# Kernel optimization log

Hardware: AMD Instinct MI355X
Metric: run time of the kernel (lower is better)

The kernel has to match this reference:

```python
import jax, jax.numpy as jnp
import numpy as np

SKIP_THRESHOLD = 0.3
NUM_HEADS = 16
TOP_K = 2


def _layernorm(x, g, b, eps=1e-6):
    m = jnp.mean(x, axis=-1, keepdims=True)
    v = jnp.var(x, axis=-1, keepdims=True)
    return (x - m) * jax.lax.rsqrt(v + eps) * g + b


def _silu(x):
    return x * jax.nn.sigmoid(x)


def _causal_dwconv(x, w):
    # x: [B,S,C], w: [k,C] depthwise causal conv
    k, S = w.shape[0], x.shape[1]
    xp = jnp.pad(x, ((0, 0), (k - 1, 0), (0, 0)))
    return sum(xp[:, i:i + S, :] * w[i] for i in range(k))


def _same_dwconv(x, w):
    k, S = w.shape[0], x.shape[1]
    pl = k // 2
    xp = jnp.pad(x, ((0, 0), (pl, k - 1 - pl), (0, 0)))
    return sum(xp[:, i:i + S, :] * w[i] for i in range(k))


def _mamba_block(x, w_in, conv_w, a_log, w_bc, w_dt, dt_bias, d_skip, w_out):
    # Selective-scan SSM (Mamba-style), O(L)
    B, S, D = x.shape
    d_inner = conv_w.shape[1]
    n = w_bc.shape[1] // 2
    xz = x @ w_in                                   # [B,S,2*d_inner]
    xc, z = xz[..., :d_inner], xz[..., d_inner:]
    xc = _silu(_causal_dwconv(xc, conv_w))
    bc = xc @ w_bc                                  # [B,S,2n]
    Bt, Ct = bc[..., :n], bc[..., n:]
    dt = jax.nn.softplus(xc * w_dt + dt_bias)       # [B,S,d_inner]
    A = -jnp.exp(a_log)                             # [d_inner]

    def step(h, inp):
        xc_t, dt_t, B_t, C_t = inp                  # [B,d_inner],[B,d_inner],[B,n],[B,n]
        decay = jnp.exp(dt_t * A)[..., None]        # [B,d_inner,1]
        h = decay * h + (dt_t * xc_t)[..., None] * B_t[:, None, :]
        y_t = jnp.einsum('bcn,bn->bc', h, C_t)
        return h, y_t

    h0 = jnp.zeros((B, d_inner, n), x.dtype)
    xs = (xc.transpose(1, 0, 2), dt.transpose(1, 0, 2),
          Bt.transpose(1, 0, 2), Ct.transpose(1, 0, 2))
    _, ys = jax.lax.scan(step, h0, xs)
    y = ys.transpose(1, 0, 2) + d_skip * xc
    return (y * _silu(z)) @ w_out


def _timecrystal_block(x, theta, w, b):
    # Energy-conserving rotation-style mixing
    return jnp.cos(theta) * x + jnp.sin(theta) * jnp.tanh(x @ w + b)


def _wlam_block(x, wq, wk, wv, wo, conv_w, nh):
    # Haar wavelet decomposition -> attention on approx coeffs -> reconstruct
    B, S, D = x.shape
    hd = D // nh
    inv = 0.7071067811865476
    xe, xo = x[:, 0::2], x[:, 1::2]
    a = (xe + xo) * inv                             # approx [B,S/2,D]
    det = (xe - xo) * inv                           # detail
    L = a.shape[1]
    q = (a @ wq).reshape(B, L, nh, hd)
    k = (a @ wk).reshape(B, L, nh, hd)
    v = (a @ wv).reshape(B, L, nh, hd)
    att = jnp.einsum('bqhd,bkhd->bhqk', q, k) * (1.0 / np.sqrt(hd))
    att = jax.nn.softmax(att, axis=-1)
    o = jnp.einsum('bhqk,bkhd->bqhd', att, v).reshape(B, L, D) @ wo
    xe2 = (o + det) * inv
    xo2 = (o - det) * inv
    y = jnp.stack([xe2, xo2], axis=2).reshape(B, S, D)
    return _same_dwconv(y, conv_w)


def _moe_block(x, wg, w1, b1, w2, b2, top_k):
    # Top-k sparse MoE; dense per-expert compute weighted by top-k gates
    B, S, D = x.shape
    E = wg.shape[1]
    xt = x.reshape(-1, D)
    logits = xt @ wg
    topv, topi = jax.lax.top_k(logits, top_k)
    w = jax.nn.softmax(topv, axis=-1)
    gates = (jax.nn.one_hot(topi, E, dtype=x.dtype) * w[..., None]).sum(axis=1)  # [T,E]
    y = jnp.zeros_like(xt)
    for e in range(E):
        h = jax.nn.gelu(xt @ w1[e] + b1[e])
        y = y + gates[:, e:e + 1] * (h @ w2[e] + b2[e])
    return y.reshape(B, S, D)


def setup_inputs() -> dict:
    key = jax.random.key(0)
    ks = jax.random.split(key, 20)
    B, S, D = 2, 2048, 1024
    DI, N, CK = 2 * D, 64, 4
    E, FF = 8, 4096
    NB = 4

    def rn(k, shape, scale=0.02):
        return jax.random.normal(k, shape, dtype=jnp.float32) * scale

    return {
        'hidden_states': jax.random.normal(ks[0], (B, S, D), jnp.float32),
        'router_w': rn(ks[1], (D, NB)),
        'router_b': jnp.zeros((NB,), jnp.float32),
        'ln_g': jnp.ones((NB, D), jnp.float32),
        'ln_b': jnp.zeros((NB, D), jnp.float32),
        'm_win': rn(ks[2], (D, 2 * DI)),
        'm_conv': rn(ks[3], (CK, DI), 0.1),
        'm_alog': jnp.zeros((DI,), jnp.float32),
        'm_wbc': rn(ks[4], (DI, 2 * N)),
        'm_wdt': rn(ks[5], (DI,)),
        'm_dtb': jnp.full((DI,), -1.0, jnp.float32),
        'm_dskip': jnp.ones((DI,), jnp.float32),
        'm_wout': rn(ks[6], (DI, D)),
        'tc_theta': jnp.array(0.5, jnp.float32),
        'tc_w': rn(ks[7], (D, D)),
        'tc_b': jnp.zeros((D,), jnp.float32),
        'w_q': rn(ks[8], (D, D)),
        'w_k': rn(ks[9], (D, D)),
        'w_v': rn(ks[10], (D, D)),
        'w_o': rn(ks[11], (D, D)),
        'wlam_conv': rn(ks[12], (4, D), 0.25),
        'moe_wg': rn(ks[13], (D, E)),
        'moe_w1': rn(ks[14], (E, D, FF)),
        'moe_b1': jnp.zeros((E, FF), jnp.float32),
        'moe_w2': rn(ks[15], (E, FF, D)),
        'moe_b2': jnp.zeros((E, D), jnp.float32),
    }


def reference(hidden_states, router_w, router_b, ln_g, ln_b,
              m_win, m_conv, m_alog, m_wbc, m_wdt, m_dtb, m_dskip, m_wout,
              tc_theta, tc_w, tc_b,
              w_q, w_k, w_v, w_o, wlam_conv,
              moe_wg, moe_w1, moe_b1, moe_w2, moe_b2):
    h = hidden_states
    # Adaptive block router: mean pool -> sigmoid scores -> hard skip mask (inference)
    pooled = jnp.mean(h, axis=1)                     # [B,D]
    scores = jax.nn.sigmoid(pooled @ router_w + router_b)  # [B,4]
    masks = (scores > SKIP_THRESHOLD).astype(h.dtype)

    h = h + masks[:, 0, None, None] * _mamba_block(
        _layernorm(h, ln_g[0], ln_b[0]), m_win, m_conv, m_alog, m_wbc,
        m_wdt, m_dtb, m_dskip, m_wout)
    h = h + masks[:, 1, None, None] * _timecrystal_block(
        _layernorm(h, ln_g[1], ln_b[1]), tc_theta, tc_w, tc_b)
    h = h + masks[:, 2, None, None] * _wlam_block(
        _layernorm(h, ln_g[2], ln_b[2]), w_q, w_k, w_v, w_o, wlam_conv, NUM_HEADS)
    h = h + masks[:, 3, None, None] * _moe_block(
        _layernorm(h, ln_g[3], ln_b[3]), moe_wg, moe_w1, moe_b1, moe_w2, moe_b2, TOP_K)
    return h
```

## Files before the change

### kernel.cpp

```cpp
#include <hip/hip_runtime.h>
#include <math.h>

#define S_LEN   2048
#define B_SZ    2
#define DM      1024
#define DI      2048
#define NST     64
#define LH      1024
#define NH      16
#define HD      64
#define TT      4096
#define NEXP    8
#define FF      4096
#define CHK     1024
#define MAXTILE 72
#define INVR2   0.7071067811865476f
#define CHUNK   128
#define NCH     16

#define OFF_POOLED 0
#define OFF_COUNTS 2048
#define OFF_CURSOR 2056
#define OFF_MASKS  2064
#define OFF_NTILE  2072
// ... 17 lines not shown
#define MB_HB   0
#define MB_W1T  4194304
#define MB_W2T  8388608
#define MB_LNB  12582912

typedef __attribute__((ext_vector_type(8))) short bf8_t;
typedef __attribute__((ext_vector_type(4))) float f4_t;

__device__ inline float b2f(unsigned short u) {
    unsigned v = (unsigned)u << 16; float f; __builtin_memcpy(&f, &v, 4); return f;
}
__device__ inline unsigned short f2b(float f) {
    unsigned u; __builtin_memcpy(&u, &f, 4);
    unsigned r = (u + 0x7fffu + ((u >> 16) & 1u)) >> 16;
    return (unsigned short)r;
}
__device__ inline void split3v(float v, unsigned short& h, unsigned short& m, unsigned short& l) {
    h = f2b(v);
    float t = v - b2f(h);
    m = f2b(t);
    float t2 = t - b2f(m);
    l = f2b(t2);
}
__device__ inline float gelu_tanh(float x) {
    float x3 = x * x * x;
    return 0.5f * x * (1.f + tanhf(0.7978845608028654f * (x + 0.044715f * x3)));
}
__device__ inline void gld16(const void* g, void* l) {
    __builtin_amdgcn_global_load_lds((const __attribute__((address_space(1))) void*)g,
                                     (__attribute__((address_space(3))) void*)l, 16, 0, 0);
}

__device__ inline float4 row_ln(float4 v, const float* __restrict__ g,
                                const float* __restrict__ bta) {
    float s1 = v.x + v.y + v.z + v.w;
    float s2 = v.x * v.x + v.y * v.y + v.z * v.z + v.w * v.w;
#pragma unroll
    for (int off = 32; off; off >>= 1) {
        s1 += __shfl_xor(s1, off);
        s2 += __shfl_xor(s2, off);
    }
    __shared__ float sh1[4], sh2[4];
    int w = threadIdx.x >> 6, lane = threadIdx.x & 63;
    if (lane == 0) { sh1[w] = s1; sh2[w] = s2; }
    __syncthreads();
    float t1 = sh1[0] + sh1[1] + sh1[2] + sh1[3];
// ... 37 lines not shown
#pragma unroll
    for (int off = 32; off; off >>= 1) {
#pragma unroll
        for (int j = 0; j < 8; ++j) p[j] += __shfl_xor(p[j], off);
    }
    __shared__ float sh[4][8];
    int w = tid >> 6, lane = tid & 63;
    if (lane == 0) {
#pragma unroll
        for (int j = 0; j < 8; ++j) sh[w][j] = p[j];
    }
    __syncthreads();
    if (tid < 8) {
        float v = sh[0][tid] + sh[1][tid] + sh[2][tid] + sh[3][tid] + rb[tid & 3];
        float sc = 1.f / (1.f + expf(-v));
        masks[tid] = (sc > 0.3f) ? 1.f : 0.f;
    }
}

__global__ __launch_bounds__(256) void ln0_copy_k(const float* __restrict__ hid,
                                                  const float* __restrict__ g,
                                                  const float* __restrict__ bta,
                                                  float* __restrict__ hout,
                                                  float* __restrict__ out) {
    int row = blockIdx.x;
    float4 v = ((const float4*)(hid + (size_t)row * DM))[threadIdx.x];
    ((float4*)(hout + (size_t)row * DM))[threadIdx.x] = v;
    float4 o = row_ln(v, g, bta);
    ((float4*)(out + (size_t)row * DM))[threadIdx.x] = o;
}

__global__ __launch_bounds__(256) void add_ln_k(float* __restrict__ h,
                                                const float* __restrict__ src,
                                                const float* __restrict__ masks, int midx,
                                                const float* __restrict__ g,
                                                const float* __restrict__ bta,
                                                float* __restrict__ out) {
    int row = blockIdx.x;
    int b = row >> 11;
    float m = masks[b * 4 + midx];
    float4 hv = ((float4*)(h + (size_t)row * DM))[threadIdx.x];
    float4 sv = ((const float4*)(src + (size_t)row * DM))[threadIdx.x];
    hv.x += m * sv.x; hv.y += m * sv.y; hv.z += m * sv.z; hv.w += m * sv.w;
    ((float4*)(h + (size_t)row * DM))[threadIdx.x] = hv;
    float4 o = row_ln(hv, g, bta);
    ((float4*)(out + (size_t)row * DM))[threadIdx.x] = o;
}

__global__ __launch_bounds__(256) void tc_ln_k(float* __restrict__ h,
                                               const float* __restrict__ ln,
                                               const float* __restrict__ gm,
                                               const float* __restrict__ tcb,
                                               const float* __restrict__ theta,
                                               const float* __restrict__ masks,
                                               const float* __restrict__ g,
                                               const float* __restrict__ bta,
                                               float* __restrict__ out) {
    int row = blockIdx.x;
    int b = row >> 11;
    float th = theta[0];
    float ct = cosf(th), st = sinf(th);
    float m = masks[b * 4 + 1];
    float4 xv = ((const float4*)(ln + (size_t)row * DM))[threadIdx.x];
    float4 gv = ((const float4*)(gm + (size_t)row * DM))[threadIdx.x];
    float4 bb = ((const float4*)tcb)[threadIdx.x];
    float4 hv = ((float4*)(h + (size_t)row * DM))[threadIdx.x];
    hv.x += m * (ct * xv.x + st * tanhf(gv.x + bb.x));
    hv.y += m * (ct * xv.y + st * tanhf(gv.y + bb.y));
    hv.z += m * (ct * xv.z + st * tanhf(gv.z + bb.z));
    hv.w += m * (ct * xv.w + st * tanhf(gv.w + bb.w));
    ((float4*)(h + (size_t)row * DM))[threadIdx.x] = hv;
    float4 o = row_ln(hv, g, bta);
    ((float4*)(out + (size_t)row * DM))[threadIdx.x] = o;
}

__global__ __launch_bounds__(256) void wpost_ln_k(float* __restrict__ h,
                                                  const float* __restrict__ o2,
                                                  const float* __restrict__ det,
                                                  const float* __restrict__ wconv,
                                                  const float* __restrict__ masks,
                                                  const float* __restrict__ g,
                                                  const float* __restrict__ bta,
                                                  float* __restrict__ out) {
    int row = blockIdx.x;
    int s = row & 2047;
    int b = row >> 11;
    float m = masks[b * 4 + 2];
    float4 acc = {0.f, 0.f, 0.f, 0.f};
#pragma unroll
    for (int t = 0; t < 4; ++t) {
        int ss = s + t - 2;
        if (ss >= 0 && ss < S_LEN) {
            int l = ss >> 1;
            size_t lr = (size_t)(b * LH + l) * DM;
            float4 ov = ((const float4*)(o2 + lr))[threadIdx.x];
            float4 dv = ((const float4*)(det + lr))[threadIdx.x];
            float sg = (ss & 1) ? -INVR2 : INVR2;
            float4 wv = ((const float4*)(wconv + (size_t)t * DM))[threadIdx.x];
            acc.x = fmaf(wv.x, INVR2 * ov.x + sg * dv.x, acc.x);
            acc.y = fmaf(wv.y, INVR2 * ov.y + sg * dv.y, acc.y);
            acc.z = fmaf(wv.z, INVR2 * ov.z + sg * dv.z, acc.z);
            acc.w = fmaf(wv.w, INVR2 * ov.w + sg * dv.w, acc.w);
        }
    }
    float4 hv = ((float4*)(h + (size_t)row * DM))[threadIdx.x];
    hv.x += m * acc.x; hv.y += m * acc.y; hv.z += m * acc.z; hv.w += m * acc.w;
    ((float4*)(h + (size_t)row * DM))[threadIdx.x] = hv;
    float4 o = row_ln(hv, g, bta);
    ((float4*)(out + (size_t)row * DM))[threadIdx.x] = o;
}

__global__ __launch_bounds__(256) void split3_k(const float* __restrict__ in,
                                                unsigned short* __restrict__ ph,
                                                unsigned short* __restrict__ pm,
                                                unsigned short* __restrict__ pl) {
    size_t f = (size_t)blockIdx.x * 256 + threadIdx.x;
    float4 v = ((const float4*)in)[f];
    ushort4 hh, mm, ll;
    split3v(v.x, hh.x, mm.x, ll.x);
    split3v(v.y, hh.y, mm.y, ll.y);
    split3v(v.z, hh.z, mm.z, ll.z);
    split3v(v.w, hh.w, mm.w, ll.w);
    ((ushort4*)ph)[f] = hh;
    ((ushort4*)pm)[f] = mm;
    ((ushort4*)pl)[f] = ll;
}

__global__ __launch_bounds__(256) void transb3_k(const float* __restrict__ in,
                                                 unsigned short* __restrict__ oh,
                                                 unsigned short* __restrict__ om,
                                                 unsigned short* __restrict__ ol,
                                                 int ldi, int ldo) {
    __shared__ float t[64][65];
    const int tid = threadIdx.x;
    const int k0 = blockIdx.x << 6, n0 = blockIdx.y << 6;
    const int rr = tid >> 4, cc = (tid & 15) << 2;
#pragma unroll
    for (int i = 0; i < 4; ++i) {
        float4 v = *(const float4*)(in + (size_t)(k0 + rr + i * 16) * ldi + n0 + cc);
        *(float4*)&t[rr + i * 16][cc] = v;
    }
    __syncthreads();
#pragma unroll
    for (int i = 0; i < 4; ++i) {
        int n = rr + i * 16;
// ... 134 lines not shown
                                            const int* __restrict__ tileC,
                                            const int* __restrict__ rtok) {
    __shared__ unsigned short As[8192];
    __shared__ unsigned short Bs[8192];
    const int tid = threadIdx.x;
    int m0 = 0;
    const int n0 = (int)blockIdx.y << 7;
    int cnt = 128, e = 0, row0 = 0;
    if constexpr (MODE >= 2) {
        if ((int)blockIdx.x >= ntile[0]) return;
        e = tileE[blockIdx.x]; row0 = tileR[blockIdx.x]; cnt = tileC[blockIdx.x];
    } else {
        m0 = (int)blockIdx.x << 7;
    }
    const unsigned short* Bp = Bt;
    if constexpr (MODE >= 2) Bp += (size_t)e << 20;
    size_t aoff[4], boff[4];
#pragma unroll
    for (int c = 0; c < 4; ++c) {
        int r = (tid >> 3) + 32 * c;
        int ks = ((tid & 7) ^ (r & 7)) << 3;
        int gr;
        if constexpr (MODE == 2)      gr = rtok[row0 + (r < cnt ? r : cnt - 1)];
        else if constexpr (MODE == 3) gr = row0 + (r < cnt ? r : cnt - 1);
        else                          gr = m0 + r;
        aoff[c] = (size_t)gr * lda + ks;
        boff[c] = (size_t)(n0 + r) * ldb + ks;
    }
    const int lane = tid & 63;
    const int w = tid >> 6, wr = w >> 1, wc = w & 1;
    const int lrow = lane & 15, lgrp = lane >> 4;
    f4_t acc[4][4];
#pragma unroll
    for (int i = 0; i < 4; ++i)
#pragma unroll
        for (int j = 0; j < 4; ++j) acc[i][j] = (f4_t){0.f, 0.f, 0.f, 0.f};
    int ard[4][2], brd[4][2];
#pragma unroll
    for (int t4 = 0; t4 < 4; ++t4)
#pragma unroll
        for (int kk = 0; kk < 2; ++kk) {
            int ra = wr * 64 + t4 * 16 + lrow;
            ard[t4][kk] = ra * 64 + (((lgrp + (kk << 2)) ^ (ra & 7)) << 3);
            int rb = wc * 64 + t4 * 16 + lrow;
            brd[t4][kk] = rb * 64 + (((lgrp + (kk << 2)) ^ (rb & 7)) << 3);
        }
    for (int k0 = 0; k0 < K; k0 += 64) {
// ... 18 lines not shown
#pragma unroll
            for (int ni = 0; ni < 4; ++ni) {
                acc[mi][ni] = __builtin_amdgcn_mfma_f32_16x16x32_bf16(af[mi][0], bfv[ni][0], acc[mi][ni], 0, 0, 0);
                acc[mi][ni] = __builtin_amdgcn_mfma_f32_16x16x32_bf16(af[mi][1], bfv[ni][1], acc[mi][ni], 0, 0, 0);
            }
    }
#pragma unroll
    for (int mi = 0; mi < 4; ++mi) {
#pragma unroll
        for (int j = 0; j < 4; ++j) {
            int lr = wr * 64 + mi * 16 + lgrp * 4 + j;
            if constexpr (MODE >= 2) { if (lr >= cnt) continue; }
#pragma unroll
            for (int ni = 0; ni < 4; ++ni) {
                int col = n0 + wc * 64 + ni * 16 + lrow;
                float vv = acc[mi][ni][j];
                if constexpr (MODE == 0) {
                    ((float*)Cv)[(size_t)(m0 + lr) * ldc + col] = vv;
                } else if constexpr (MODE == 1) {
                    ((unsigned short*)Cv)[(size_t)(m0 + lr) * ldc + col] = f2b(vv);
                } else if constexpr (MODE == 2) {
                    float bz = bias[(size_t)e * FF + fofs + col];
                    ((unsigned short*)Cv)[(size_t)(row0 + lr) * ldc + col] = f2b(gelu_tanh(vv + bz));
                } else {
                    ((float*)Cv)[(size_t)(row0 + lr) * ldc + col] += vv;
                }
            }
        }
    }
}

__global__ __launch_bounds__(256) void gemm_f32(const float* __restrict__ A, int lda,
                                                const float* __restrict__ B, int ldb,
                                                float* __restrict__ C, int ldc, int K) {
    __shared__ float As[16][68];
    __shared__ float Bs[16][68];
    const int tid = threadIdx.x;
    const int tx = tid & 15, ty = tid >> 4;
    const int m0 = blockIdx.x * 64, n0 = blockIdx.y * 64;
    const int la_r = tid >> 2, la_k = (tid & 3) << 2;
    const int lb_r = tid >> 4, lb_n = (tid & 15) << 2;
    float acc[4][4] = {};
    for (int k0 = 0; k0 < K; k0 += 16) {
        float4 av = *(const float4*)(A + (size_t)(m0 + la_r) * lda + k0 + la_k);
        float4 bv = *(const float4*)(B + (size_t)(k0 + lb_r) * ldb + n0 + lb_n);
        __syncthreads();
        As[la_k + 0][la_r] = av.x; As[la_k + 1][la_r] = av.y;
        As[la_k + 2][la_r] = av.z; As[la_k + 3][la_r] = av.w;
        *(float4*)&Bs[lb_r][lb_n] = bv;
        __syncthreads();
#pragma unroll
        for (int kk = 0; kk < 16; ++kk) {
            float4 a4 = *(const float4*)&As[kk][ty << 2];
            float4 b4 = *(const float4*)&Bs[kk][tx << 2];
            float aa[4] = {a4.x, a4.y, a4.z, a4.w};
            float bb[4] = {b4.x, b4.y, b4.z, b4.w};
#pragma unroll
            for (int i = 0; i < 4; ++i)
#pragma unroll
                for (int j = 0; j < 4; ++j)
                    acc[i][j] = fmaf(aa[i], bb[j], acc[i][j]);
        }
    }
#pragma unroll
    for (int i = 0; i < 4; ++i) {
        int m = m0 + (ty << 2) + i;
        float4 o;
        o.x = acc[i][0]; o.y = acc[i][1]; o.z = acc[i][2]; o.w = acc[i][3];
        *(float4*)(C + (size_t)m * ldc + n0 + (tx << 2)) = o;
    }
}

__global__ __launch_bounds__(256) void mamba_conv_k(const float* __restrict__ xz,
                                                    const float* __restrict__ cw,
                                                    float* __restrict__ xc) {
    size_t i = (size_t)blockIdx.x * 256 + threadIdx.x;
    int c = (int)(i & (DI - 1));
    size_t row = i >> 11;
    int s = (int)(row & (S_LEN - 1));
    float acc = 0.f;
#pragma unroll
    for (int t = 0; t < 4; ++t) {
        int ss = s - 3 + t;
        if (ss >= 0) acc = fmaf(cw[t * DI + c], xz[(row - 3 + t) * 4096 + c], acc);
    }
    float sg = 1.f / (1.f + expf(-acc));
    xc[i] = acc * sg;
}

__global__ __launch_bounds__(256) void scan1_k(const float* __restrict__ xc,
                                               const float* __restrict__ bc,
                                               const float* __restrict__ alog,
                                               const float* __restrict__ wdt,
// ... 97 lines not shown
        float coef = dtv * xcv;
        float y = 0.f;
#pragma unroll
        for (int n4 = 0; n4 < 16; ++n4) {
            float4 bv = *(const float4*)&Bs[s][n4 << 2];
            float4 cv = *(const float4*)&Cs[s][n4 << 2];
            float h0 = fmaf(decay, hs[n4 * 4 + 0], coef * bv.x);
            float h1 = fmaf(decay, hs[n4 * 4 + 1], coef * bv.y);
            float h2 = fmaf(decay, hs[n4 * 4 + 2], coef * bv.z);
            float h3 = fmaf(decay, hs[n4 * 4 + 3], coef * bv.w);
            hs[n4 * 4 + 0] = h0; hs[n4 * 4 + 1] = h1;
            hs[n4 * 4 + 2] = h2; hs[n4 * 4 + 3] = h3;
            y = fmaf(h0, cv.x, y); y = fmaf(h1, cv.y, y);
            y = fmaf(h2, cv.z, y); y = fmaf(h3, cv.w, y);
        }
        y = fmaf(skipc, xcv, y);
        float z = zp[(size_t)s * 4096];
        float sz = z / (1.f + expf(-z));
        xcp[(size_t)s * DI] = y * sz;
    }
}

__global__ __launch_bounds__(256) void wsplit_k(const float* __restrict__ ln,
                                                float* __restrict__ a, float* __restrict__ det) {
    size_t f = (size_t)blockIdx.x * 256 + threadIdx.x;
    int d4 = (int)(f & 255);
    size_t l = f >> 8;
    size_t b = l >> 10;
    size_t li = l & 1023;
    const float4* ln4 = (const float4*)ln;
    float4 xe = ln4[(b * S_LEN + 2 * li) * 256 + d4];
    float4 xo = ln4[(b * S_LEN + 2 * li + 1) * 256 + d4];
    float4 av, dv;
    av.x = (xe.x + xo.x) * INVR2; dv.x = (xe.x - xo.x) * INVR2;
    av.y = (xe.y + xo.y) * INVR2; dv.y = (xe.y - xo.y) * INVR2;
    av.z = (xe.z + xo.z) * INVR2; dv.z = (xe.z - xo.z) * INVR2;
    av.w = (xe.w + xo.w) * INVR2; dv.w = (xe.w - xo.w) * INVR2;
    ((float4*)a)[f] = av;
    ((float4*)det)[f] = dv;
}

__global__ __launch_bounds__(256) void wlam_attn_k(const float* __restrict__ q,
                                                   const float* __restrict__ k,
                                                   const float* __restrict__ v,
                                                   float* __restrict__ o) {
    __shared__ float Qt[64][68];
    __shared__ float KPt[64][68];
    __shared__ float Vs[64][68];
    const int tid = threadIdx.x;
    const int b = blockIdx.z, hh = blockIdx.y;
    const int q0 = blockIdx.x << 6;
    const int tx = tid & 15, ty = tid >> 4;
    const int sr = tid & 63, sc4 = (tid >> 6) << 4;
    {
        const float* qp = q + ((size_t)(b * LH + q0 + sr)) * DM + hh * HD + sc4;
        float4 v0 = *(const float4*)qp;
        float4 v1 = *(const float4*)(qp + 4);
        float4 v2 = *(const float4*)(qp + 8);
        float4 v3 = *(const float4*)(qp + 12);
        Qt[sc4 + 0][sr] = v0.x;  Qt[sc4 + 1][sr] = v0.y;  Qt[sc4 + 2][sr] = v0.z;  Qt[sc4 + 3][sr] = v0.w;
        Qt[sc4 + 4][sr] = v1.x;  Qt[sc4 + 5][sr] = v1.y;  Qt[sc4 + 6][sr] = v1.z;  Qt[sc4 + 7][sr] = v1.w;
        Qt[sc4 + 8][sr] = v2.x;  Qt[sc4 + 9][sr] = v2.y;  Qt[sc4 + 10][sr] = v2.z; Qt[sc4 + 11][sr] = v2.w;
        Qt[sc4 + 12][sr] = v3.x; Qt[sc4 + 13][sr] = v3.y; Qt[sc4 + 14][sr] = v3.z; Qt[sc4 + 15][sr] = v3.w;
    }
    float mrow[4] = {-INFINITY, -INFINITY, -INFINITY, -INFINITY};
    float lrow[4] = {0.f, 0.f, 0.f, 0.f};
    float oacc[4][4] = {};
    for (int c0 = 0; c0 < LH; c0 += 64) {
        __syncthreads();
        {
            const float* kp = k + ((size_t)(b * LH + c0 + sr)) * DM + hh * HD + sc4;
            float4 v0 = *(const float4*)kp;
            float4 v1 = *(const float4*)(kp + 4);
            float4 v2 = *(const float4*)(kp + 8);
            float4 v3 = *(const float4*)(kp + 12);
            KPt[sc4 + 0][sr] = v0.x;  KPt[sc4 + 1][sr] = v0.y;  KPt[sc4 + 2][sr] = v0.z;  KPt[sc4 + 3][sr] = v0.w;
            KPt[sc4 + 4][sr] = v1.x;  KPt[sc4 + 5][sr] = v1.y;  KPt[sc4 + 6][sr] = v1.z;  KPt[sc4 + 7][sr] = v1.w;
            KPt[sc4 + 8][sr] = v2.x;  KPt[sc4 + 9][sr] = v2.y;  KPt[sc4 + 10][sr] = v2.z; KPt[sc4 + 11][sr] = v2.w;
            KPt[sc4 + 12][sr] = v3.x; KPt[sc4 + 13][sr] = v3.y; KPt[sc4 + 14][sr] = v3.z; KPt[sc4 + 15][sr] = v3.w;
            const float* vp = v + ((size_t)(b * LH + c0 + sr)) * DM + hh * HD + sc4;
            *(float4*)&Vs[sr][sc4 + 0]  = *(const float4*)vp;
            *(float4*)&Vs[sr][sc4 + 4]  = *(const float4*)(vp + 4);
            *(float4*)&Vs[sr][sc4 + 8]  = *(const float4*)(vp + 8);
            *(float4*)&Vs[sr][sc4 + 12] = *(const float4*)(vp + 12);
        }
        __syncthreads();
        float s[4][4] = {};
#pragma unroll
        for (int d = 0; d < 64; ++d) {
            float4 a4 = *(const float4*)&Qt[d][ty << 2];
            float4 b4 = *(const float4*)&KPt[d][tx << 2];
// ... 36 lines not shown
            oacc[i][0] *= corr[i]; oacc[i][1] *= corr[i];
            oacc[i][2] *= corr[i]; oacc[i][3] *= corr[i];
        }
        __syncthreads();
#pragma unroll
        for (int j = 0; j < 4; ++j) {
            float4 pv; pv.x = s[0][j]; pv.y = s[1][j]; pv.z = s[2][j]; pv.w = s[3][j];
            *(float4*)&KPt[(tx << 2) + j][ty << 2] = pv;
        }
        __syncthreads();
#pragma unroll
        for (int kk = 0; kk < 64; ++kk) {
            float4 pa = *(const float4*)&KPt[kk][ty << 2];
            float4 vb = *(const float4*)&Vs[kk][tx << 2];
            float aa[4] = {pa.x, pa.y, pa.z, pa.w};
            float bb[4] = {vb.x, vb.y, vb.z, vb.w};
#pragma unroll
            for (int i = 0; i < 4; ++i)
#pragma unroll
                for (int j = 0; j < 4; ++j)
                    oacc[i][j] = fmaf(aa[i], bb[j], oacc[i][j]);
        }
    }
#pragma unroll
    for (int i = 0; i < 4; ++i) {
        float inv = 1.f / lrow[i];
        float4 ov;
        ov.x = oacc[i][0] * inv; ov.y = oacc[i][1] * inv;
        ov.z = oacc[i][2] * inv; ov.w = oacc[i][3] * inv;
        *(float4*)(o + ((size_t)(b * LH + q0 + (ty << 2) + i)) * DM + hh * HD + (tx << 2)) = ov;
    }
}

__global__ __launch_bounds__(256) void moe_gate_k(const float* __restrict__ X,
                                                  const float* __restrict__ wg,
                                                  int* __restrict__ toke,
                                                  float* __restrict__ tokw) {
    const int wv = threadIdx.x >> 6, lane = threadIdx.x & 63;
    const int t = blockIdx.x * 4 + wv;
    const float* x = X + (size_t)t * DM;
    float acc[8] = {0, 0, 0, 0, 0, 0, 0, 0};
    for (int d = lane; d < DM; d += 64) {
        float xv = x[d];
        const float4* wg4 = (const float4*)(wg + (size_t)d * 8);
        float4 wa = wg4[0], wb = wg4[1];
        acc[0] = fmaf(xv, wa.x, acc[0]); acc[1] = fmaf(xv, wa.y, acc[1]);
        acc[2] = fmaf(xv, wa.z, acc[2]); acc[3] = fmaf(xv, wa.w, acc[3]);
        acc[4] = fmaf(xv, wb.x, acc[4]); acc[5] = fmaf(xv, wb.y, acc[5]);
        acc[6] = fmaf(xv, wb.z, acc[6]); acc[7] = fmaf(xv, wb.w, acc[7]);
    }
#pragma unroll
    for (int off = 32; off; off >>= 1) {
#pragma unroll
        for (int j = 0; j < 8; ++j) acc[j] += __shfl_xor(acc[j], off);
    }
    if (lane == 0) {
        int i0 = 0; float v0 = acc[0];
#pragma unroll
        for (int e2 = 1; e2 < 8; ++e2) if (acc[e2] > v0) { v0 = acc[e2]; i0 = e2; }
        int i1 = -1; float v1 = -INFINITY;
#pragma unroll
        for (int e2 = 0; e2 < 8; ++e2) if (e2 != i0 && acc[e2] > v1) { v1 = acc[e2]; i1 = e2; }
        float r = expf(v1 - v0);
        float den = 1.f + r;
        toke[2 * t] = i0; toke[2 * t + 1] = i1;
        tokw[2 * t] = 1.f / den; tokw[2 * t + 1] = r / den;
    }
}

__global__ __launch_bounds__(256) void cast16_k(const float* __restrict__ in,
                                                unsigned short* __restrict__ out) {
    size_t f = (size_t)blockIdx.x * 256 + threadIdx.x;
    float4 v = ((const float4*)in)[f];
    ushort4 o;
    o.x = f2b(v.x); o.y = f2b(v.y); o.z = f2b(v.z); o.w = f2b(v.w);
    ((ushort4*)out)[f] = o;
}

__global__ __launch_bounds__(256) void moe_count_k(const int* __restrict__ toke, int* __restrict__ counts) {
    int t = blockIdx.x * 256 + threadIdx.x;
    atomicAdd(&counts[toke[2 * t]], 1);
    atomicAdd(&counts[toke[2 * t + 1]], 1);
}

__global__ void moe_tiles_k(const int* __restrict__ counts, int* __restrict__ ntile,
                            int* __restrict__ eoff, int* __restrict__ tileE,
                            int* __restrict__ tileR, int* __restrict__ tileC) {
    if (threadIdx.x == 0 && blockIdx.x == 0) {
        int off = 0, nt = 0;
        for (int e = 0; e < NEXP; ++e) {
            eoff[e] = off;
            int c = counts[e];
            for (int r = 0; r < c; r += 128) {
                tileE[nt] = e;
                tileR[nt] = off + r;
                tileC[nt] = (c - r < 128) ? (c - r) : 128;
                ++nt;
            }
            off += c;
        }
        ntile[0] = nt;
    }
}

__global__ __launch_bounds__(256) void moe_place_k(const int* __restrict__ toke,
                                                   const float* __restrict__ tokw,
                                                   const int* __restrict__ eoff,
                                                   int* __restrict__ cursor,
                                                   int* __restrict__ rtok,
                                                   float* __restrict__ rgate,
                                                   int* __restrict__ rexp,
                                                   int* __restrict__ rowof) {
    int t = blockIdx.x * 256 + threadIdx.x;
#pragma unroll
    for (int kk = 0; kk < 2; ++kk) {
        int e = toke[2 * t + kk];
        float wv = tokw[2 * t + kk];
        int r = eoff[e] + atomicAdd(&cursor[e], 1);
        rtok[r] = t; rgate[r] = wv; rexp[r] = e;
        rowof[2 * t + kk] = r;
    }
}

__global__ __launch_bounds__(256) void moe_init_k(float* __restrict__ P,
                                                  const float* __restrict__ b2,
                                                  const int* __restrict__ rexp) {
    int r = blockIdx.x;
    int e = rexp[r];
    float4 bv = ((const float4*)(b2 + (size_t)e * DM))[threadIdx.x];
    ((float4*)(P + (size_t)r * DM))[threadIdx.x] = bv;
}

__global__ __launch_bounds__(256) void moe_combine_k(float* __restrict__ h,
                                                     const float* __restrict__ P,
                                                     const int* __restrict__ rowof,
                                                     const float* __restrict__ rgate,
                                                     const float* __restrict__ masks) {
    int t = blockIdx.x;
    int r0 = rowof[2 * t], r1 = rowof[2 * t + 1];
    float g0 = rgate[r0], g1 = rgate[r1];
    float m = masks[(t >> 11) * 4 + 3];
    float4 a = ((const float4*)(P + (size_t)r0 * DM))[threadIdx.x];
    float4 bq = ((const float4*)(P + (size_t)r1 * DM))[threadIdx.x];
    float4* h4 = (float4*)(h + (size_t)t * DM);
    float4 hv = h4[threadIdx.x];
    hv.x += m * (g0 * a.x + g1 * bq.x);
    hv.y += m * (g0 * a.y + g1 * bq.y);
    hv.z += m * (g0 * a.z + g1 * bq.z);
    hv.w += m * (g0 * a.w + g1 * bq.w);
    h4[threadIdx.x] = hv;
}

extern "C" void kernel_launch(void* const* d_in, const int* in_sizes, int n_in,
// ... 19 lines not shown
    const float* w_k       = (const float*)d_in[17];
    const float* w_v       = (const float*)d_in[18];
    const float* w_o       = (const float*)d_in[19];
    const float* wlam_cv   = (const float*)d_in[20];
    const float* moe_wg    = (const float*)d_in[21];
    const float* moe_w1    = (const float*)d_in[22];
    const float* moe_b1    = (const float*)d_in[23];
    const float* moe_w2    = (const float*)d_in[24];
    const float* moe_b2    = (const float*)d_in[25];
    float* h = (float*)d_out;
    float* w = (float*)d_ws;
    unsigned short* BIGH = (unsigned short*)(w + OFF_BIG);
    unsigned short* XCU  = (unsigned short*)(w + OFF_XC);
    unsigned short* OUTU = (unsigned short*)(w + OFF_OUT);
#define UPB(F) (BIGH + 2 * (size_t)(F))
#define UPX(F) (XCU  + 2 * (size_t)(F))
#define UPO(F) (OUTU + 2 * (size_t)(F))

    hipMemsetAsync(d_ws, 0, 2064 * sizeof(float), stream);

    pooled_k<<<dim3(4, 2, 16), 256, 0, stream>>>(hidden, w + OFF_POOLED);
    router_k<<<1, 256, 0, stream>>>(w + OFF_POOLED, router_w, router_b, w + OFF_MASKS);

    ln0_copy_k<<<TT, 256, 0, stream>>>(hidden, ln_g + 0 * DM, ln_b + 0 * DM, h, w + OFF_LN);
    split3_k<<<4096, 256, 0, stream>>>(w + OFF_LN, UPX(0), UPX(2097152), UPX(4194304));
    transb3_k<<<dim3(16, 64), 256, 0, stream>>>(m_win, UPO(0), UPO(2097152), UPX(6291456), 4096, 1024);
    mmx3_k<<<dim3(32, 32), 256, 0, stream>>>(UPX(0), UPX(2097152), UPX(4194304),
                                             UPO(0), UPO(2097152), UPX(6291456),
                                             w + OFF_BIG, 1024, 1024, 4096, 1024);
    mamba_conv_k<<<32768, 256, 0, stream>>>(w + OFF_BIG, m_conv, w + OFF_XC);
    gemm_f32<<<dim3(64, 2), 256, 0, stream>>>(w + OFF_XC, DI, m_wbc, 128, w + OFF_BC, 128, DI);
    scan1_k<<<dim3(8, NCH, B_SZ), 256, 0, stream>>>(w + OFF_XC, w + OFF_BC,
                                                    m_alog, m_wdt, m_dtb,
                                                    w + OFF_LN, w + OFF_PPROD);
    scan2_k<<<1024, 256, 0, stream>>>(w + OFF_LN, w + OFF_PPROD, w + OFF_OUT);
    scan3_k<<<dim3(8, NCH, B_SZ), 256, 0, stream>>>(w + OFF_XC, w + OFF_BC, w + OFF_BIG,
                                                    m_alog, m_wdt, m_dtb, m_dskip,
                                                    w + OFF_OUT);
    split3_k<<<8192, 256, 0, stream>>>(w + OFF_XC, UPB(0), UPB(4194304), UPB(8388608));
    transb3_k<<<dim3(32, 16), 256, 0, stream>>>(m_wout, UPB(12582912), UPB(13631488), UPB(14680064), 1024, 2048);
    mmx3_k<<<dim3(32, 8), 256, 0, stream>>>(UPB(0), UPB(4194304), UPB(8388608),
                                            UPB(12582912), UPB(13631488), UPB(14680064),
                                            w + OFF_OUT, 2048, 2048, 1024, 2048);
    add_ln_k<<<TT, 256, 0, stream>>>(h, w + OFF_OUT, w + OFF_MASKS, 0,
                                     ln_g + 1 * DM, ln_b + 1 * DM, w + OFF_LN);

    split3_k<<<4096, 256, 0, stream>>>(w + OFF_LN, UPB(0), UPB(2097152), UPB(4194304));
    transb3_k<<<dim3(16, 16), 256, 0, stream>>>(tc_w, UPB(6291456), UPB(6815744), UPB(7340032), 1024, 1024);
    mmx3_k<<<dim3(32, 8), 256, 0, stream>>>(UPB(0), UPB(2097152), UPB(4194304),
                                            UPB(6291456), UPB(6815744), UPB(7340032),
                                            w + OFF_OUT, 1024, 1024, 1024, 1024);
    tc_ln_k<<<TT, 256, 0, stream>>>(h, w + OFF_LN, w + OFF_OUT, tc_b, tc_theta, w + OFF_MASKS,
                                    ln_g + 2 * DM, ln_b + 2 * DM, w + OFF_LN);

    float* wa   = w + OFF_BIG;
    float* wdet = w + OFF_BIG + 2097152;
    wsplit_k<<<2048, 256, 0, stream>>>(w + OFF_LN, wa, wdet);
    split3_k<<<2048, 256, 0, stream>>>(wa, UPB(4194304), UPB(5242880), UPB(6291456));
    transb3_k<<<dim3(16, 16), 256, 0, stream>>>(w_q, UPB(7340032),  UPB(7864320),  UPB(8388608),  1024, 1024);
    transb3_k<<<dim3(16, 16), 256, 0, stream>>>(w_k, UPB(8912896),  UPB(9437184),  UPB(9961472),  1024, 1024);
    transb3_k<<<dim3(16, 16), 256, 0, stream>>>(w_v, UPB(10485760), UPB(11010048), UPB(11534336), 1024, 1024);
    transb3_k<<<dim3(16, 16), 256, 0, stream>>>(w_o, UPB(12058624), UPB(12582912), UPB(13107200), 1024, 1024);
    float* wq_ = w + OFF_XC;
    float* wk_ = w + OFF_XC + 2097152;
    float* wv_ = w + OFF_XC + 4194304;
    float* wo_ = w + OFF_XC + 6291456;
    mmx3_k<<<dim3(16, 8), 256, 0, stream>>>(UPB(4194304), UPB(5242880), UPB(6291456),
                                            UPB(7340032), UPB(7864320), UPB(8388608),
                                            wq_, 1024, 1024, 1024, 1024);
    mmx3_k<<<dim3(16, 8), 256, 0, stream>>>(UPB(4194304), UPB(5242880), UPB(6291456),
                                            UPB(8912896), UPB(9437184), UPB(9961472),
                                            wk_, 1024, 1024, 1024, 1024);
    mmx3_k<<<dim3(16, 8), 256, 0, stream>>>(UPB(4194304), UPB(5242880), UPB(6291456),
                                            UPB(10485760), UPB(11010048), UPB(11534336),
                                            wv_, 1024, 1024, 1024, 1024);
    wlam_attn_k<<<dim3(16, NH, B_SZ), 256, 0, stream>>>(wq_, wk_, wv_, wo_);
    split3_k<<<2048, 256, 0, stream>>>(wo_, UPB(13631488), UPB(14680064), UPB(15728640));
    mmx3_k<<<dim3(16, 8), 256, 0, stream>>>(UPB(13631488), UPB(14680064), UPB(15728640),
                                            UPB(12058624), UPB(12582912), UPB(13107200),
                                            w + OFF_OUT, 1024, 1024, 1024, 1024);
    wpost_ln_k<<<TT, 256, 0, stream>>>(h, w + OFF_OUT, wdet, wlam_cv, w + OFF_MASKS,
                                       ln_g + 3 * DM, ln_b + 3 * DM, w + OFF_LN);

    moe_gate_k<<<1024, 256, 0, stream>>>(w + OFF_LN, moe_wg, (int*)(w + OFF_TOKE), w + OFF_TOKW);
    cast16_k<<<4096, 256, 0, stream>>>(w + OFF_LN, UPB(MB_LNB));
    moe_count_k<<<16, 256, 0, stream>>>((const int*)(w + OFF_TOKE), (int*)(w + OFF_COUNTS));
    moe_tiles_k<<<1, 64, 0, stream>>>((const int*)(w + OFF_COUNTS), (int*)(w + OFF_NTILE),
                                      (int*)(w + OFF_EOFF), (int*)(w + OFF_TILEE),
                                      (int*)(w + OFF_TILER), (int*)(w + OFF_TILEC));
    moe_place_k<<<16, 256, 0, stream>>>((const int*)(w + OFF_TOKE), w + OFF_TOKW,
                                        (const int*)(w + OFF_EOFF), (int*)(w + OFF_CURSOR),
                                        (int*)(w + OFF_RTOK), w + OFF_RGATE,
                                        (int*)(w + OFF_REXP), (int*)(w + OFF_ROWOF));
    moe_init_k<<<8192, 256, 0, stream>>>(w + OFF_XC, moe_b2, (const int*)(w + OFF_REXP));
    for (int ci = 0; ci < 4; ++ci) {
        transb_k<<<dim3(16, 16, NEXP), 256, 0, stream>>>(moe_w1 + (size_t)ci * CHK,
                                                         UPB(MB_W1T),
                                                         FF, 1024, (long)DM * FF, 1024L * 1024L);
        transb_k<<<dim3(16, 16, NEXP), 256, 0, stream>>>(moe_w2 + (size_t)ci * CHK * DM,
                                                         UPB(MB_W2T),
                                                         DM, 1024, (long)FF * DM, 1024L * 1024L);
        mm_k<2><<<dim3(MAXTILE, 8), 256, 0, stream>>>(UPB(MB_LNB),
                                                      UPB(MB_W1T),
                                                      UPB(MB_HB),
                                                      1024, 1024, 1024, 1024,
                                                      moe_b1, ci * CHK,
                                                      (const int*)(w + OFF_NTILE), (const int*)(w + OFF_TILEE),
                                                      (const int*)(w + OFF_TILER), (const int*)(w + OFF_TILEC),
                                                      (const int*)(w + OFF_RTOK));
        mm_k<3><<<dim3(MAXTILE, 8), 256, 0, stream>>>(UPB(MB_HB),
                                                      UPB(MB_W2T),
                                                      w + OFF_XC, 1024, 1024, 1024, 1024,
                                                      nullptr, 0,
                                                      (const int*)(w + OFF_NTILE), (const int*)(w + OFF_TILEE),
                                                      (const int*)(w + OFF_TILER), (const int*)(w + OFF_TILEC),
                                                      nullptr);
    }
    moe_combine_k<<<4096, 256, 0, stream>>>(h, w + OFF_XC, (const int*)(w + OFF_ROWOF),
                                            w + OFF_RGATE, w + OFF_MASKS);
#undef UPB
#undef UPX
#undef UPO
}
```

Before: 1.839 ms.

## Fuse bf16 splits into producers, split-K scan GEMM, split-KV attention

Several elementwise kernels go away. The bf16 three-way split and the cast are folded into the layernorm and wavelet producer kernels. The MoE bias init is folded into the first down-projection epilogue, which now writes instead of accumulating. The small B/C projection GEMM, which ran on only 128 blocks, is split along K into 8 slabs and followed by a reduction kernel. Wavelet attention is split into two KV halves whose partial results are merged by a new kernel that also does the split. This trades extra partial-buffer traffic for fewer launches and more parallelism.

```diff
diff --git a/kernel.cpp b/kernel.cpp
--- a/kernel.cpp
+++ b/kernel.cpp
@@ -63,6 +63,12 @@
     float t2 = t - b2f(m);
     l = f2b(t2);
 }
+__device__ inline void split3q(float4 v, ushort4& h4, ushort4& m4, ushort4& l4) {
+    split3v(v.x, h4.x, m4.x, l4.x);
+    split3v(v.y, h4.y, m4.y, l4.y);
+    split3v(v.z, h4.z, m4.z, l4.z);
+    split3v(v.w, h4.w, m4.w, l4.w);
+}
 __device__ inline float gelu_tanh(float x) {
     float x3 = x * x * x;
     return 0.5f * x * (1.f + tanhf(0.7978845608028654f * (x + 0.044715f * x3)));
@@ -146,12 +152,19 @@
                                                   const float* __restrict__ g,
                                                   const float* __restrict__ bta,
                                                   float* __restrict__ hout,
-                                                  float* __restrict__ out) {
+                                                  unsigned short* __restrict__ ph,
+                                                  unsigned short* __restrict__ pm,
+                                                  unsigned short* __restrict__ pl) {
     int row = blockIdx.x;
     float4 v = ((const float4*)(hid + (size_t)row * DM))[threadIdx.x];
     ((float4*)(hout + (size_t)row * DM))[threadIdx.x] = v;
     float4 o = row_ln(v, g, bta);
-    ((float4*)(out + (size_t)row * DM))[threadIdx.x] = o;
+    ushort4 h4, m4, l4;
+    split3q(o, h4, m4, l4);
+    size_t f = (size_t)row * 256 + threadIdx.x;
+    ((ushort4*)ph)[f] = h4;
+    ((ushort4*)pm)[f] = m4;
+    ((ushort4*)pl)[f] = l4;
 }
 
 __global__ __launch_bounds__(256) void add_ln_k(float* __restrict__ h,
@@ -159,7 +172,10 @@
                                                 const float* __restrict__ masks, int midx,
                                                 const float* __restrict__ g,
                                                 const float* __restrict__ bta,
-                                                float* __restrict__ out) {
+                                                float* __restrict__ out,
+                                                unsigned short* __restrict__ ph,
+                                                unsigned short* __restrict__ pm,
+                                                unsigned short* __restrict__ pl) {
     int row = blockIdx.x;
     int b = row >> 11;
     float m = masks[b * 4 + midx];
@@ -169,6 +185,12 @@
     ((float4*)(h + (size_t)row * DM))[threadIdx.x] = hv;
     float4 o = row_ln(hv, g, bta);
     ((float4*)(out + (size_t)row * DM))[threadIdx.x] = o;
+    ushort4 h4, m4, l4;
+    split3q(o, h4, m4, l4);
+    size_t f = (size_t)row * 256 + threadIdx.x;
+    ((ushort4*)ph)[f] = h4;
+    ((ushort4*)pm)[f] = m4;
+    ((ushort4*)pl)[f] = l4;
 }
 
 __global__ __launch_bounds__(256) void tc_ln_k(float* __restrict__ h,
@@ -205,7 +227,8 @@
                                                   const float* __restrict__ masks,
                                                   const float* __restrict__ g,
                                                   const float* __restrict__ bta,
-                                                  float* __restrict__ out) {
+                                                  float* __restrict__ out,
+                                                  unsigned short* __restrict__ outb) {
     int row = blockIdx.x;
     int s = row & 2047;
     int b = row >> 11;
@@ -232,6 +255,9 @@
     ((float4*)(h + (size_t)row * DM))[threadIdx.x] = hv;
     float4 o = row_ln(hv, g, bta);
     ((float4*)(out + (size_t)row * DM))[threadIdx.x] = o;
+    ushort4 ob;
+    ob.x = f2b(o.x); ob.y = f2b(o.y); ob.z = f2b(o.z); ob.w = f2b(o.w);
+    ((ushort4*)(outb))[(size_t)row * 256 + threadIdx.x] = ob;
 }
 
 __global__ __launch_bounds__(256) void split3_k(const float* __restrict__ in,
@@ -241,10 +267,7 @@
     size_t f = (size_t)blockIdx.x * 256 + threadIdx.x;
     float4 v = ((const float4*)in)[f];
     ushort4 hh, mm, ll;
-    split3v(v.x, hh.x, mm.x, ll.x);
-    split3v(v.y, hh.y, mm.y, ll.y);
-    split3v(v.z, hh.z, mm.z, ll.z);
-    split3v(v.w, hh.w, mm.w, ll.w);
+    split3q(v, hh, mm, ll);
     ((ushort4*)ph)[f] = hh;
     ((ushort4*)pm)[f] = mm;
     ((ushort4*)pl)[f] = ll;
@@ -425,7 +448,7 @@
         int ks = ((tid & 7) ^ (r & 7)) << 3;
         int gr;
         if constexpr (MODE == 2)      gr = rtok[row0 + (r < cnt ? r : cnt - 1)];
-        else if constexpr (MODE == 3) gr = row0 + (r < cnt ? r : cnt - 1);
+        else if constexpr (MODE >= 3) gr = row0 + (r < cnt ? r : cnt - 1);
         else                          gr = m0 + r;
         aoff[c] = (size_t)gr * lda + ks;
         boff[c] = (size_t)(n0 + r) * ldb + ks;
@@ -490,26 +513,30 @@
                 } else if constexpr (MODE == 2) {
                     float bz = bias[(size_t)e * FF + fofs + col];
                     ((unsigned short*)Cv)[(size_t)(row0 + lr) * ldc + col] = f2b(gelu_tanh(vv + bz));
+                } else if constexpr (MODE == 3) {
+                    ((float*)Cv)[(size_t)(row0 + lr) * ldc + col] += vv;
                 } else {
-                    ((float*)Cv)[(size_t)(row0 + lr) * ldc + col] += vv;
+                    ((float*)Cv)[(size_t)(row0 + lr) * ldc + col] = vv + bias[(size_t)e * DM + col];
                 }
             }
         }
     }
 }
 
-__global__ __launch_bounds__(256) void gemm_f32(const float* __restrict__ A, int lda,
-                                                const float* __restrict__ B, int ldb,
-                                                float* __restrict__ C, int ldc, int K) {
+__global__ __launch_bounds__(256) void gemmsk_f32(const float* __restrict__ A, int lda,
+                                                  const float* __restrict__ B, int ldb,
+                                                  float* __restrict__ P, int ldc, int Kslab) {
     __shared__ float As[16][68];
     __shared__ float Bs[16][68];
     const int tid = threadIdx.x;
     const int tx = tid & 15, ty = tid >> 4;
     const int m0 = blockIdx.x * 64, n0 = blockIdx.y * 64;
+    const int kbeg = blockIdx.z * Kslab, kend = kbeg + Kslab;
+    P += (size_t)blockIdx.z * 4096 * 128;
     const int la_r = tid >> 2, la_k = (tid & 3) << 2;
     const int lb_r = tid >> 4, lb_n = (tid & 15) << 2;
     float acc[4][4] = {};
-    for (int k0 = 0; k0 < K; k0 += 16) {
+    for (int k0 = kbeg; k0 < kend; k0 += 16) {
         float4 av = *(const float4*)(A + (size_t)(m0 + la_r) * lda + k0 + la_k);
         float4 bv = *(const float4*)(B + (size_t)(k0 + lb_r) * ldb + n0 + lb_n);
         __syncthreads();
@@ -535,8 +562,17 @@
         int m = m0 + (ty << 2) + i;
         float4 o;
         o.x = acc[i][0]; o.y = acc[i][1]; o.z = acc[i][2]; o.w = acc[i][3];
-        *(float4*)(C + (size_t)m * ldc + n0 + (tx << 2)) = o;
-    }
+        *(float4*)(P + (size_t)m * ldc + n0 + (tx << 2)) = o;
+    }
+}
+
+__global__ __launch_bounds__(256) void wbc_red_k(const float* __restrict__ part,
+                                                 float* __restrict__ bc) {
+    size_t i = (size_t)blockIdx.x * 256 + threadIdx.x;
+    float s = 0.f;
+#pragma unroll
+    for (int z = 0; z < 8; ++z) s += part[(size_t)z * 524288 + i];
+    bc[i] = s;
 }
 
 __global__ __launch_bounds__(256) void mamba_conv_k(const float* __restrict__ xz,
@@ -680,7 +716,10 @@
 }
 
 __global__ __launch_bounds__(256) void wsplit_k(const float* __restrict__ ln,
-                                                float* __restrict__ a, float* __restrict__ det) {
+                                                unsigned short* __restrict__ ah,
+                                                unsigned short* __restrict__ am,
+                                                unsigned short* __restrict__ al,
+                                                float* __restrict__ det) {
     size_t f = (size_t)blockIdx.x * 256 + threadIdx.x;
     int d4 = (int)(f & 255);
     size_t l = f >> 8;
@@ -694,19 +733,26 @@
     av.y = (xe.y + xo.y) * INVR2; dv.y = (xe.y - xo.y) * INVR2;
     av.z = (xe.z + xo.z) * INVR2; dv.z = (xe.z - xo.z) * INVR2;
     av.w = (xe.w + xo.w) * INVR2; dv.w = (xe.w - xo.w) * INVR2;
-    ((float4*)a)[f] = av;
+    ushort4 h4, m4, l4;
+    split3q(av, h4, m4, l4);
+    ((ushort4*)ah)[f] = h4;
+    ((ushort4*)am)[f] = m4;
+    ((ushort4*)al)[f] = l4;
     ((float4*)det)[f] = dv;
 }
 
 __global__ __launch_bounds__(256) void wlam_attn_k(const float* __restrict__ q,
                                                    const float* __restrict__ k,
                                                    const float* __restrict__ v,
-                                                   float* __restrict__ o) {
+                                                   float* __restrict__ o0,
+                                                   float* __restrict__ o1,
+                                                   float* __restrict__ ml) {
     __shared__ float Qt[64][68];
     __shared__ float KPt[64][68];
     __shared__ float Vs[64][68];
     const int tid = threadIdx.x;
-    const int b = blockIdx.z, hh = blockIdx.y;
+    const int b = blockIdx.z >> 1, half = blockIdx.z & 1;
+    const int hh = blockIdx.y;
     const int q0 = blockIdx.x << 6;
     const int tx = tid & 15, ty = tid >> 4;
     const int sr = tid & 63, sc4 = (tid >> 6) << 4;
@@ -724,7 +770,8 @@
     float mrow[4] = {-INFINITY, -INFINITY, -INFINITY, -INFINITY};
     float lrow[4] = {0.f, 0.f, 0.f, 0.f};
     float oacc[4][4] = {};
-    for (int c0 = 0; c0 < LH; c0 += 64) {
+    const int c0beg = half << 9;
+    for (int c0 = c0beg; c0 < c0beg + 512; c0 += 64) {
         __syncthreads();
         {
             const float* kp = k + ((size_t)(b * LH + c0 + sr)) * DM + hh * HD + sc4;
@@ -807,14 +854,49 @@
                     oacc[i][j] = fmaf(aa[i], bb[j], oacc[i][j]);
         }
     }
+    float* op = half ? o1 : o0;
 #pragma unroll
     for (int i = 0; i < 4; ++i) {
-        float inv = 1.f / lrow[i];
+        int rrow = q0 + (ty << 2) + i;
         float4 ov;
-        ov.x = oacc[i][0] * inv; ov.y = oacc[i][1] * inv;
-        ov.z = oacc[i][2] * inv; ov.w = oacc[i][3] * inv;
-        *(float4*)(o + ((size_t)(b * LH + q0 + (ty << 2) + i)) * DM + hh * HD + (tx << 2)) = ov;
-    }
+        ov.x = oacc[i][0]; ov.y = oacc[i][1]; ov.z = oacc[i][2]; ov.w = oacc[i][3];
+        *(float4*)(op + ((size_t)(b * LH + rrow)) * DM + hh * HD + (tx << 2)) = ov;
+        if (tx == 0) {
+            size_t mi = (size_t)half * 65536 + ((size_t)(b * LH + rrow) * NH + hh) * 2;
+            ml[mi] = mrow[i];
+            ml[mi + 1] = lrow[i];
+        }
+    }
+}
+
+__global__ __launch_bounds__(256) void attn_merge_k(const float* __restrict__ o0,
+                                                    const float* __restrict__ o1,
+                                                    const float* __restrict__ ml,
+                                                    unsigned short* __restrict__ ph,
+                                                    unsigned short* __restrict__ pm,
+                                                    unsigned short* __restrict__ pl) {
+    int row = blockIdx.x;
+    int t = threadIdx.x;
+    int hh = t >> 4;
+    size_t idx = ((size_t)row * NH + hh) * 2;
+    float m0 = ml[idx], l0 = ml[idx + 1];
+    float m1 = ml[65536 + idx], l1 = ml[65536 + idx + 1];
+    float m = fmaxf(m0, m1);
+    float w0 = expf(m0 - m), w1 = expf(m1 - m);
+    float inv = 1.f / (l0 * w0 + l1 * w1);
+    float4 a = ((const float4*)(o0 + (size_t)row * DM))[t];
+    float4 bv = ((const float4*)(o1 + (size_t)row * DM))[t];
+    float4 o;
+    o.x = (a.x * w0 + bv.x * w1) * inv;
+    o.y = (a.y * w0 + bv.y * w1) * inv;
+    o.z = (a.z * w0 + bv.z * w1) * inv;
+    o.w = (a.w * w0 + bv.w * w1) * inv;
+    ushort4 h4, m4, l4;
+    split3q(o, h4, m4, l4);
+    size_t f = (size_t)row * 256 + t;
+    ((ushort4*)ph)[f] = h4;
+    ((ushort4*)pm)[f] = m4;
+    ((ushort4*)pl)[f] = l4;
 }
 
 __global__ __launch_bounds__(256) void moe_gate_k(const float* __restrict__ X,
@@ -853,15 +935,6 @@
     }
 }
 
-__global__ __launch_bounds__(256) void cast16_k(const float* __restrict__ in,
-                                                unsigned short* __restrict__ out) {
-    size_t f = (size_t)blockIdx.x * 256 + threadIdx.x;
-    float4 v = ((const float4*)in)[f];
-    ushort4 o;
-    o.x = f2b(v.x); o.y = f2b(v.y); o.z = f2b(v.z); o.w = f2b(v.w);
-    ((ushort4*)out)[f] = o;
-}
-
 __global__ __launch_bounds__(256) void moe_count_k(const int* __restrict__ toke, int* __restrict__ counts) {
     int t = blockIdx.x * 256 + threadIdx.x;
     atomicAdd(&counts[toke[2 * t]], 1);
@@ -905,15 +978,6 @@
         rtok[r] = t; rgate[r] = wv; rexp[r] = e;
         rowof[2 * t + kk] = r;
     }
-}
-
-__global__ __launch_bounds__(256) void moe_init_k(float* __restrict__ P,
-                                                  const float* __restrict__ b2,
-                                                  const int* __restrict__ rexp) {
-    int r = blockIdx.x;
-    int e = rexp[r];
-    float4 bv = ((const float4*)(b2 + (size_t)e * DM))[threadIdx.x];
-    ((float4*)(P + (size_t)r * DM))[threadIdx.x] = bv;
 }
 
 __global__ __launch_bounds__(256) void moe_combine_k(float* __restrict__ h,
@@ -979,14 +1043,15 @@
     pooled_k<<<dim3(4, 2, 16), 256, 0, stream>>>(hidden, w + OFF_POOLED);
     router_k<<<1, 256, 0, stream>>>(w + OFF_POOLED, router_w, router_b, w + OFF_MASKS);
 
-    ln0_copy_k<<<TT, 256, 0, stream>>>(hidden, ln_g + 0 * DM, ln_b + 0 * DM, h, w + OFF_LN);
-    split3_k<<<4096, 256, 0, stream>>>(w + OFF_LN, UPX(0), UPX(2097152), UPX(4194304));
+    ln0_copy_k<<<TT, 256, 0, stream>>>(hidden, ln_g + 0 * DM, ln_b + 0 * DM, h,
+                                       UPX(0), UPX(2097152), UPX(4194304));
     transb3_k<<<dim3(16, 64), 256, 0, stream>>>(m_win, UPO(0), UPO(2097152), UPX(6291456), 4096, 1024);
     mmx3_k<<<dim3(32, 32), 256, 0, stream>>>(UPX(0), UPX(2097152), UPX(4194304),
                                              UPO(0), UPO(2097152), UPX(6291456),
                                              w + OFF_BIG, 1024, 1024, 4096, 1024);
     mamba_conv_k<<<32768, 256, 0, stream>>>(w + OFF_BIG, m_conv, w + OFF_XC);
-    gemm_f32<<<dim3(64, 2), 256, 0, stream>>>(w + OFF_XC, DI, m_wbc, 128, w + OFF_BC, 128, DI);
+    gemmsk_f32<<<dim3(64, 2, 8), 256, 0, stream>>>(w + OFF_XC, DI, m_wbc, 128, w + OFF_LN, 128, 256);
+    wbc_red_k<<<2048, 256, 0, stream>>>(w + OFF_LN, w + OFF_BC);
     scan1_k<<<dim3(8, NCH, B_SZ), 256, 0, stream>>>(w + OFF_XC, w + OFF_BC,
                                                     m_alog, m_wdt, m_dtb,
                                                     w + OFF_LN, w + OFF_PPROD);
@@ -1000,9 +1065,9 @@
                                             UPB(12582912), UPB(13631488), UPB(14680064),
                                             w + OFF_OUT, 2048, 2048, 1024, 2048);
     add_ln_k<<<TT, 256, 0, stream>>>(h, w + OFF_OUT, w + OFF_MASKS, 0,
-                                     ln_g + 1 * DM, ln_b + 1 * DM, w + OFF_LN);
-
-    split3_k<<<4096, 256, 0, stream>>>(w + OFF_LN, UPB(0), UPB(2097152), UPB(4194304));
+                                     ln_g + 1 * DM, ln_b + 1 * DM, w + OFF_LN,
+                                     UPB(0), UPB(2097152), UPB(4194304));
+
     transb3_k<<<dim3(16, 16), 256, 0, stream>>>(tc_w, UPB(6291456), UPB(6815744), UPB(7340032), 1024, 1024);
     mmx3_k<<<dim3(32, 8), 256, 0, stream>>>(UPB(0), UPB(2097152), UPB(4194304),
                                             UPB(6291456), UPB(6815744), UPB(7340032),
@@ -1010,10 +1075,8 @@
     tc_ln_k<<<TT, 256, 0, stream>>>(h, w + OFF_LN, w + OFF_OUT, tc_b, tc_theta, w + OFF_MASKS,
                                     ln_g + 2 * DM, ln_b + 2 * DM, w + OFF_LN);
 
-    float* wa   = w + OFF_BIG;
-    float* wdet = w + OFF_BIG + 2097152;
-    wsplit_k<<<2048, 256, 0, stream>>>(w + OFF_LN, wa, wdet);
-    split3_k<<<2048, 256, 0, stream>>>(wa, UPB(4194304), UPB(5242880), UPB(6291456));
+    float* wdet = w + OFF_BIG;
+    wsplit_k<<<2048, 256, 0, stream>>>(w + OFF_LN, UPB(4194304), UPB(5242880), UPB(6291456), wdet);
     transb3_k<<<dim3(16, 16), 256, 0, stream>>>(w_q, UPB(7340032),  UPB(7864320),  UPB(8388608),  1024, 1024);
     transb3_k<<<dim3(16, 16), 256, 0, stream>>>(w_k, UPB(8912896),  UPB(9437184),  UPB(9961472),  1024, 1024);
     transb3_k<<<dim3(16, 16), 256, 0, stream>>>(w_v, UPB(10485760), UPB(11010048), UPB(11534336), 1024, 1024);
@@ -1021,7 +1084,9 @@
     float* wq_ = w + OFF_XC;
     float* wk_ = w + OFF_XC + 2097152;
     float* wv_ = w + OFF_XC + 4194304;
-    float* wo_ = w + OFF_XC + 6291456;
+    float* wo0 = w + OFF_XC + 6291456;
+    float* wo1 = w + OFF_OUT;
+    float* wml = w + OFF_OUT + 2097152;
     mmx3_k<<<dim3(16, 8), 256, 0, stream>>>(UPB(4194304), UPB(5242880), UPB(6291456),
                                             UPB(7340032), UPB(7864320), UPB(8388608),
                                             wq_, 1024, 1024, 1024, 1024);
@@ -1031,16 +1096,17 @@
     mmx3_k<<<dim3(16, 8), 256, 0, stream>>>(UPB(4194304), UPB(5242880), UPB(6291456),
                                             UPB(10485760), UPB(11010048), UPB(11534336),
                                             wv_, 1024, 1024, 1024, 1024);
-    wlam_attn_k<<<dim3(16, NH, B_SZ), 256, 0, stream>>>(wq_, wk_, wv_, wo_);
-    split3_k<<<2048, 256, 0, stream>>>(wo_, UPB(13631488), UPB(14680064), UPB(15728640));
+    wlam_attn_k<<<dim3(16, NH, B_SZ * 2), 256, 0, stream>>>(wq_, wk_, wv_, wo0, wo1, wml);
+    attn_merge_k<<<2048, 256, 0, stream>>>(wo0, wo1, wml,
+                                           UPB(13631488), UPB(14680064), UPB(15728640));
     mmx3_k<<<dim3(16, 8), 256, 0, stream>>>(UPB(13631488), UPB(14680064), UPB(15728640),
                                             UPB(12058624), UPB(12582912), UPB(13107200),
                                             w + OFF_OUT, 1024, 1024, 1024, 1024);
     wpost_ln_k<<<TT, 256, 0, stream>>>(h, w + OFF_OUT, wdet, wlam_cv, w + OFF_MASKS,
-                                       ln_g + 3 * DM, ln_b + 3 * DM, w + OFF_LN);
+                                       ln_g + 3 * DM, ln_b + 3 * DM, w + OFF_LN,
+                                       UPB(MB_LNB));
 
     moe_gate_k<<<1024, 256, 0, stream>>>(w + OFF_LN, moe_wg, (int*)(w + OFF_TOKE), w + OFF_TOKW);
-    cast16_k<<<4096, 256, 0, stream>>>(w + OFF_LN, UPB(MB_LNB));
     moe_count_k<<<16, 256, 0, stream>>>((const int*)(w + OFF_TOKE), (int*)(w + OFF_COUNTS));
     moe_tiles_k<<<1, 64, 0, stream>>>((const int*)(w + OFF_COUNTS), (int*)(w + OFF_NTILE),
                                       (int*)(w + OFF_EOFF), (int*)(w + OFF_TILEE),
@@ -1049,7 +1115,6 @@
                                         (const int*)(w + OFF_EOFF), (int*)(w + OFF_CURSOR),
                                         (int*)(w + OFF_RTOK), w + OFF_RGATE,
                                         (int*)(w + OFF_REXP), (int*)(w + OFF_ROWOF));
-    moe_init_k<<<8192, 256, 0, stream>>>(w + OFF_XC, moe_b2, (const int*)(w + OFF_REXP));
     for (int ci = 0; ci < 4; ++ci) {
         transb_k<<<dim3(16, 16, NEXP), 256, 0, stream>>>(moe_w1 + (size_t)ci * CHK,
                                                          UPB(MB_W1T),
@@ -1057,21 +1122,27 @@
         transb_k<<<dim3(16, 16, NEXP), 256, 0, stream>>>(moe_w2 + (size_t)ci * CHK * DM,
                                                          UPB(MB_W2T),
                                                          DM, 1024, (long)FF * DM, 1024L * 1024L);
-        mm_k<2><<<dim3(MAXTILE, 8), 256, 0, stream>>>(UPB(MB_LNB),
-                                                      UPB(MB_W1T),
-                                                      UPB(MB_HB),
+        mm_k<2><<<dim3(MAXTILE, 8), 256, 0, stream>>>(UPB(MB_LNB), UPB(MB_W1T), UPB(MB_HB),
                                                       1024, 1024, 1024, 1024,
                                                       moe_b1, ci * CHK,
                                                       (const int*)(w + OFF_NTILE), (const int*)(w + OFF_TILEE),
                                                       (const int*)(w + OFF_TILER), (const int*)(w + OFF_TILEC),
                                                       (const int*)(w + OFF_RTOK));
-        mm_k<3><<<dim3(MAXTILE, 8), 256, 0, stream>>>(UPB(MB_HB),
-                                                      UPB(MB_W2T),
-                                                      w + OFF_XC, 1024, 1024, 1024, 1024,
-                                                      nullptr, 0,
-                                                      (const int*)(w + OFF_NTILE), (const int*)(w + OFF_TILEE),
-                                                      (const int*)(w + OFF_TILER), (const int*)(w + OFF_TILEC),
-                                                      nullptr);
+        if (ci == 0) {
+            mm_k<4><<<dim3(MAXTILE, 8), 256, 0, stream>>>(UPB(MB_HB), UPB(MB_W2T),
+                                                          w + OFF_XC, 1024, 1024, 1024, 1024,
+                                                          moe_b2, 0,
+                                                          (const int*)(w + OFF_NTILE), (const int*)(w + OFF_TILEE),
+                                                          (const int*)(w + OFF_TILER), (const int*)(w + OFF_TILEC),
+                                                          nullptr);
+        } else {
+            mm_k<3><<<dim3(MAXTILE, 8), 256, 0, stream>>>(UPB(MB_HB), UPB(MB_W2T),
+                                                          w + OFF_XC, 1024, 1024, 1024, 1024,
+                                                          nullptr, 0,
+                                                          (const int*)(w + OFF_NTILE), (const int*)(w + OFF_TILEE),
+                                                          (const int*)(w + OFF_TILER), (const int*)(w + OFF_TILEC),
+                                                          nullptr);
+        }
     }
     moe_combine_k<<<4096, 256, 0, stream>>>(h, w + OFF_XC, (const int*)(w + OFF_ROWOF),
                                             w + OFF_RGATE, w + OFF_MASKS);
```

Result: faster. 1.726 ms (-6.1%).
